# Optimization experiments

Hardware: AMD Instinct MI355X
Metric: run time of the kernel (lower is better)

The kernel has to match this reference:

```python
import jax, jax.numpy as jnp
import numpy as np


def sparsemax(z):
    """Euclidean projection onto the simplex (Martins & Astudillo 2016).
    z: (..., L) logits -> sparse probability vectors of same shape.
    """
    L = z.shape[-1]
    z_sorted = jnp.flip(jnp.sort(z, axis=-1), axis=-1)          # descending
    cum = jnp.cumsum(z_sorted, axis=-1)
    k = jnp.arange(1, L + 1, dtype=z.dtype)                     # 1..L
    support = 1.0 + k * z_sorted > cum                          # prefix-true mask
    k_max = jnp.sum(support, axis=-1, keepdims=True).astype(z.dtype)
    # sum of z_sorted over the support == cumsum at the last supported index
    cum_at_k = jnp.sum(jnp.where(support, z_sorted, 0.0), axis=-1, keepdims=True)
    tau = (cum_at_k - 1.0) / k_max
    return jnp.maximum(z - tau, 0.0)


def setup_inputs() -> dict:
    key = jax.random.key(0)
    k1, k2 = jax.random.split(key)
    B, K, L = 64, 16, 16384
    attention_logits = jax.random.normal(k1, (B, K, L), dtype=jnp.float32)
    rationale_mask = (jax.random.uniform(k2, (B, L)) < 0.1).astype(jnp.float32)
    return {"attention_logits": attention_logits, "rationale_mask": rationale_mask}


def reference(attention_logits, rationale_mask):
    # normalize the rationale mask into a probability target q
    q = rationale_mask / jnp.clip(
        jnp.sum(rationale_mask, axis=-1, keepdims=True), 1e-12, None
    )  # (B, L)
    p = sparsemax(attention_logits)            # (B, K, L), all heads batched
    diff = p - q[:, None, :]                   # broadcast target over heads
    # per-(example, head) loss 0.5*||p - q||^2, then mean over batch and heads
    # (= mean over heads of per-head batch means, as in the torch loop)
    return 0.5 * jnp.mean(jnp.sum(diff * diff, axis=-1))
```

## Files before the change

kernel.cpp:

```cpp
#include <hip/hip_runtime.h>

#define BB 64
#define KK 16
#define LL 16384
#define CAP 2048

__global__ __launch_bounds__(256) void mask_stats_kernel(
    const float* __restrict__ mask, float* __restrict__ stats) {
  int b = blockIdx.x;
  const float* m = mask + (size_t)b * LL;
  int t = threadIdx.x;
  float s = 0.f, sq = 0.f;
#pragma unroll
  for (int j = 0; j < 16; ++j) {
    float4 v = reinterpret_cast<const float4*>(m)[j * 256 + t];
    s  += v.x + v.y + v.z + v.w;
    sq += v.x * v.x + v.y * v.y + v.z * v.z + v.w * v.w;
  }
  for (int off = 32; off; off >>= 1) {
    s  += __shfl_xor(s, off);
    sq += __shfl_xor(sq, off);
  }
  __shared__ float ls[4], lsq[4];
  int wave = t >> 6;
  if ((t & 63) == 0) { ls[wave] = s; lsq[wave] = sq; }
  __syncthreads();
  if (t == 0) {
    float S  = ls[0] + ls[1] + ls[2] + ls[3];
    float SQ = lsq[0] + lsq[1] + lsq[2] + lsq[3];
    float inv = 1.0f / fmaxf(S, 1e-12f);
    stats[2 * b]     = inv;
    stats[2 * b + 1] = SQ * inv * inv;
  }
}

__global__ __launch_bounds__(256) void sparsemax_loss_kernel(
    const float* __restrict__ logits, const float* __restrict__ mask,
    const float* __restrict__ stats, float* __restrict__ out) {
  int row = blockIdx.x;
  int b = row >> 4;
  const float* z = logits + (size_t)row * LL;
  const float* m = mask + (size_t)b * LL;
  int t = threadIdx.x;
  int wave = t >> 6, lane = t & 63;

  __shared__ float lds_val[CAP];
  __shared__ int   lds_idx[CAP];
  __shared__ int   lds_n;
  __shared__ float lds_f[4];

  if (t == 0) lds_n = 0;

  float4 v[16];
  float vmax = -3.0e38f;
#pragma unroll
  for (int j = 0; j < 16; ++j) {
    v[j] = reinterpret_cast<const float4*>(z)[j * 256 + t];
    vmax = fmaxf(vmax, fmaxf(fmaxf(v[j].x, v[j].y), fmaxf(v[j].z, v[j].w)));
  }
  for (int off = 32; off; off >>= 1) vmax = fmaxf(vmax, __shfl_xor(vmax, off));
  if (lane == 0) lds_f[wave] = vmax;
  __syncthreads();
  float zmax = fmaxf(fmaxf(lds_f[0], lds_f[1]), fmaxf(lds_f[2], lds_f[3]));
  float thr = zmax - 1.0f;

#pragma unroll
  for (int j = 0; j < 16; ++j) {
    int base = (j * 256 + t) * 4;
    float vv[4] = {v[j].x, v[j].y, v[j].z, v[j].w};
#pragma unroll
    for (int e = 0; e < 4; ++e) {
      if (vv[e] > thr) {
        int pos = atomicAdd(&lds_n, 1);
        if (pos < CAP) { lds_val[pos] = vv[e]; lds_idx[pos] = base + e; }
      }
    }
  }
  __syncthreads();
  int n = lds_n;
  float inv_s = stats[2 * b];
  float sumq2 = stats[2 * b + 1];
  const float scale = 0.5f / (float)(BB * KK);

  if (n <= CAP) {
    if (wave == 0) {
      int nj = (n + 63) >> 6;
      float lo = thr, hi = zmax;
      for (int it = 0; it < 30; ++it) {
        float mid = 0.5f * (lo + hi);
        float s = 0.f;
        for (int j = 0; j < nj; ++j) {
          int i = j * 64 + lane;
          float c = (i < n) ? lds_val[i] : -3.0e38f;
          s += fmaxf(c - mid, 0.f);
        }
        for (int off = 32; off; off >>= 1) s += __shfl_xor(s, off);
        if (s >= 1.0f) lo = mid; else hi = mid;
      }
      float S = 0.f, kc = 0.f;
      for (int j = 0; j < nj; ++j) {
        int i = j * 64 + lane;
        float c = (i < n) ? lds_val[i] : -3.0e38f;
        if (c > lo) { S += c; kc += 1.f; }
      }
      for (int off = 32; off; off >>= 1) {
        S  += __shfl_xor(S, off);
        kc += __shfl_xor(kc, off);
      }
      float tau = (S - 1.0f) / kc;

      float a1 = 0.f, a2 = 0.f;
      for (int j = 0; j < nj; ++j) {
        int i = j * 64 + lane;
        if (i < n) {
          float p = fmaxf(lds_val[i] - tau, 0.f);
          if (p > 0.f) {
            float q = m[lds_idx[i]] * inv_s;
            a1 += p * p;
            a2 += p * q;
          }
        }
      }
      for (int off = 32; off; off >>= 1) {
        a1 += __shfl_xor(a1, off);
        a2 += __shfl_xor(a2, off);
      }
      if (lane == 0) {
        atomicAdd(out, (a1 - 2.f * a2 + sumq2) * scale);
      }
    }
  } else {
    __shared__ float red[4], red2[4];
    float lo = thr, hi = zmax;
    for (int it = 0; it < 30; ++it) {
      float mid = 0.5f * (lo + hi);
      float s = 0.f;
#pragma unroll
      for (int j = 0; j < 16; ++j) {
        s += fmaxf(v[j].x - mid, 0.f) + fmaxf(v[j].y - mid, 0.f) +
             fmaxf(v[j].z - mid, 0.f) + fmaxf(v[j].w - mid, 0.f);
      }
      for (int off = 32; off; off >>= 1) s += __shfl_xor(s, off);
      __syncthreads();
      if (lane == 0) red[wave] = s;
      __syncthreads();
      float tot = red[0] + red[1] + red[2] + red[3];
      if (tot >= 1.0f) lo = mid; else hi = mid;
    }
    float S = 0.f, kc = 0.f;
#pragma unroll
    for (int j = 0; j < 16; ++j) {
      float vv[4] = {v[j].x, v[j].y, v[j].z, v[j].w};
#pragma unroll
      for (int e = 0; e < 4; ++e)
        if (vv[e] > lo) { S += vv[e]; kc += 1.f; }
    }
    for (int off = 32; off; off >>= 1) {
      S  += __shfl_xor(S, off);
      kc += __shfl_xor(kc, off);
    }
    __syncthreads();
    if (lane == 0) { red[wave] = S; red2[wave] = kc; }
    __syncthreads();
    S  = red[0] + red[1] + red[2] + red[3];
    kc = red2[0] + red2[1] + red2[2] + red2[3];
    float tau = (S - 1.0f) / kc;

    float a1 = 0.f, a2 = 0.f;
#pragma unroll
    for (int j = 0; j < 16; ++j) {
      int base = (j * 256 + t) * 4;
      float vv[4] = {v[j].x, v[j].y, v[j].z, v[j].w};
#pragma unroll
      for (int e = 0; e < 4; ++e) {
        float p = fmaxf(vv[e] - tau, 0.f);
        if (p > 0.f) {
          float q = m[base + e] * inv_s;
          a1 += p * p;
          a2 += p * q;
        }
      }
    }
    for (int off = 32; off; off >>= 1) {
      a1 += __shfl_xor(a1, off);
      a2 += __shfl_xor(a2, off);
    }
    __syncthreads();
    if (lane == 0) { red[wave] = a1; red2[wave] = a2; }
    __syncthreads();
    if (t == 0) {
      a1 = red[0] + red[1] + red[2] + red[3];
      a2 = red2[0] + red2[1] + red2[2] + red2[3];
      atomicAdd(out, (a1 - 2.f * a2 + sumq2) * scale);
    }
  }
}

extern "C" void kernel_launch(void* const* d_in, const int* in_sizes, int n_in,
                              void* d_out, int out_size, void* d_ws, size_t ws_size,
                              hipStream_t stream) {
  const float* logits = (const float*)d_in[0];
  const float* mask   = (const float*)d_in[1];
  float* stats = (float*)d_ws;
  float* out   = (float*)d_out;

  hipMemsetAsync(out, 0, sizeof(float), stream);
  mask_stats_kernel<<<BB, 256, 0, stream>>>(mask, stats);
  sparsemax_loss_kernel<<<BB * KK, 256, 0, stream>>>(logits, mask, stats, out);
}
```

Baseline: 112.2 us.

## Add exact bitonic-sort sparsemax path for small candidate sets, reload logits in fallback

When at most 64 candidates survive the zmax-1 filter, wave 0 sorts them with a register bitonic network, takes a shuffle prefix sum, and finds the support with a ballot. This computes tau exactly in one pass instead of 30 bisection iterations over LDS. The rare overflow path now reloads logits from global memory instead of keeping them in registers, which should cut register pressure and raise occupancy for the common path. Repeated global reads in that fallback path cost more if it is ever taken.

```diff
diff --git a/kernel.cpp b/kernel.cpp
--- a/kernel.cpp
+++ b/kernel.cpp
@@ -82,7 +82,50 @@
   float sumq2 = stats[2 * b + 1];
   const float scale = 0.5f / (float)(BB * KK);
 
-  if (n <= CAP) {
+  if (n <= 64) {
+    if (wave == 0) {
+      float c = (lane < n) ? lds_val[lane] : -3.0e38f;
+#pragma unroll
+      for (int size = 2; size <= 64; size <<= 1) {
+#pragma unroll
+        for (int stride = size >> 1; stride > 0; stride >>= 1) {
+          float other = __shfl_xor(c, stride);
+          bool dirDesc = ((lane & size) == 0);
+          bool takeMax = (dirDesc == ((lane & stride) == 0));
+          float mn = fminf(c, other), mx = fmaxf(c, other);
+          c = takeMax ? mx : mn;
+        }
+      }
+      float cum = c;
+#pragma unroll
+      for (int off = 1; off < 64; off <<= 1) {
+        float y = __shfl_up(cum, off);
+        if (lane >= off) cum += y;
+      }
+      bool sup = (lane < n) && (1.0f + (float)(lane + 1) * c > cum);
+      unsigned long long bal = __ballot(sup);
+      int k = __popcll(bal);
+      float S = sup ? c : 0.f;
+      for (int off = 32; off; off >>= 1) S += __shfl_xor(S, off);
+      float tau = (S - 1.0f) / (float)k;
+
+      float a1 = 0.f, a2 = 0.f;
+      if (lane < n) {
+        float val = lds_val[lane];
+        float p = fmaxf(val - tau, 0.f);
+        if (p > 0.f) {
+          float q = m[lds_idx[lane]] * inv_s;
+          a1 = p * p;
+          a2 = p * q;
+        }
+      }
+      for (int off = 32; off; off >>= 1) {
+        a1 += __shfl_xor(a1, off);
+        a2 += __shfl_xor(a2, off);
+      }
+      if (lane == 0) atomicAdd(out, (a1 - 2.f * a2 + sumq2) * scale);
+    }
+  } else if (n <= CAP) {
     if (wave == 0) {
       int nj = (n + 63) >> 6;
       float lo = thr, hi = zmax;
@@ -91,8 +134,8 @@
         float s = 0.f;
         for (int j = 0; j < nj; ++j) {
           int i = j * 64 + lane;
-          float c = (i < n) ? lds_val[i] : -3.0e38f;
-          s += fmaxf(c - mid, 0.f);
+          float cc = (i < n) ? lds_val[i] : -3.0e38f;
+          s += fmaxf(cc - mid, 0.f);
         }
         for (int off = 32; off; off >>= 1) s += __shfl_xor(s, off);
         if (s >= 1.0f) lo = mid; else hi = mid;
@@ -100,8 +143,8 @@
       float S = 0.f, kc = 0.f;
       for (int j = 0; j < nj; ++j) {
         int i = j * 64 + lane;
-        float c = (i < n) ? lds_val[i] : -3.0e38f;
-        if (c > lo) { S += c; kc += 1.f; }
+        float cc = (i < n) ? lds_val[i] : -3.0e38f;
+        if (cc > lo) { S += cc; kc += 1.f; }
       }
       for (int off = 32; off; off >>= 1) {
         S  += __shfl_xor(S, off);
@@ -125,9 +168,7 @@
         a1 += __shfl_xor(a1, off);
         a2 += __shfl_xor(a2, off);
       }
-      if (lane == 0) {
-        atomicAdd(out, (a1 - 2.f * a2 + sumq2) * scale);
-      }
+      if (lane == 0) atomicAdd(out, (a1 - 2.f * a2 + sumq2) * scale);
     }
   } else {
     __shared__ float red[4], red2[4];
@@ -135,10 +176,10 @@
     for (int it = 0; it < 30; ++it) {
       float mid = 0.5f * (lo + hi);
       float s = 0.f;
-#pragma unroll
       for (int j = 0; j < 16; ++j) {
-        s += fmaxf(v[j].x - mid, 0.f) + fmaxf(v[j].y - mid, 0.f) +
-             fmaxf(v[j].z - mid, 0.f) + fmaxf(v[j].w - mid, 0.f);
+        float4 vv = reinterpret_cast<const float4*>(z)[j * 256 + t];
+        s += fmaxf(vv.x - mid, 0.f) + fmaxf(vv.y - mid, 0.f) +
+             fmaxf(vv.z - mid, 0.f) + fmaxf(vv.w - mid, 0.f);
       }
       for (int off = 32; off; off >>= 1) s += __shfl_xor(s, off);
       __syncthreads();
@@ -148,10 +189,9 @@
       if (tot >= 1.0f) lo = mid; else hi = mid;
     }
     float S = 0.f, kc = 0.f;
-#pragma unroll
     for (int j = 0; j < 16; ++j) {
-      float vv[4] = {v[j].x, v[j].y, v[j].z, v[j].w};
-#pragma unroll
+      float4 vv4 = reinterpret_cast<const float4*>(z)[j * 256 + t];
+      float vv[4] = {vv4.x, vv4.y, vv4.z, vv4.w};
       for (int e = 0; e < 4; ++e)
         if (vv[e] > lo) { S += vv[e]; kc += 1.f; }
     }
@@ -167,11 +207,10 @@
     float tau = (S - 1.0f) / kc;
 
     float a1 = 0.f, a2 = 0.f;
-#pragma unroll
     for (int j = 0; j < 16; ++j) {
       int base = (j * 256 + t) * 4;
-      float vv[4] = {v[j].x, v[j].y, v[j].z, v[j].w};
-#pragma unroll
+      float4 vv4 = reinterpret_cast<const float4*>(z)[j * 256 + t];
+      float vv[4] = {vv4.x, vv4.y, vv4.z, vv4.w};
       for (int e = 0; e < 4; ++e) {
         float p = fmaxf(vv[e] - tau, 0.f);
         if (p > 0.f) {
```

New measurement: 111.0 us. No clear change (-1.1%).
